# Kernel optimization log

Hardware: AMD Instinct MI355X
Metric: run time of the kernel (lower is better)

## Reference

```python
import jax, jax.numpy as jnp
import numpy as np

N = 2_097_152          # n_transitions = n_envs * buffer_size
GAMMA = 0.99
GAE_LAMBDA = 0.95
CLIP_EPS = 0.2
NORM_ADVANTAGES = True


def setup_inputs() -> dict:
    key = jax.random.key(0)
    ks = jax.random.split(key, 7)
    f = lambda k: jax.random.normal(k, (N, 1), dtype=jnp.float32)
    return {
        "rewards": f(ks[0]),
        "values": f(ks[1]),
        "next_values": f(ks[2]),
        "log_probs": -jnp.abs(f(ks[3])),       # log-probs are <= 0
        "old_log_probs": -jnp.abs(f(ks[4])),
        "terminated": jax.random.randint(ks[5], (N, 1), 0, 2).astype(bool),
        "truncated": jax.random.randint(ks[6], (N, 1), 0, 2).astype(bool),
    }


def reference(rewards, values, next_values, log_probs, old_log_probs,
              terminated, truncated):
    dtype = rewards.dtype
    dones = jnp.logical_or(terminated, truncated)
    not_term = 1.0 - terminated.astype(dtype)          # [N,1]
    not_done = 1.0 - dones.astype(dtype)               # [N,1]

    # TD residuals: delta_n = r_n + gamma * (1 - terminated_n) * V(s'_n) - V(s_n)
    deltas = rewards + GAMMA * not_term * next_values - values   # [N,1]

    # Reverse GAE recurrence (the torch Python for-loop, fused into one scan):
    # adv_n = (1 - done_n) * gamma * lambda * adv_{n+1} + delta_n
    coef = not_done[:, 0] * (GAMMA * GAE_LAMBDA)       # [N]

    def step(adv, cd):
        c, d = cd
        adv = c * adv + d
        return adv, adv

    _, advantages = jax.lax.scan(step, jnp.zeros((), dtype),
                                 (coef, deltas[:, 0]), reverse=True)
    advantages = advantages[:, None]                   # [N,1]

    lambda_returns = advantages + values               # [N,1]

    if NORM_ADVANTAGES:
        # torch .std() is the unbiased (ddof=1) estimator
        adv_n = (advantages - advantages.mean()) / (
            jnp.std(advantages, ddof=1) + 1e-9)
    else:
        adv_n = advantages

    # PPO clipped surrogate, per-sample (the .mean() is a trivial reduction)
    ratio = jnp.exp(log_probs - old_log_probs)
    clamped = jnp.clip(ratio, 1.0 - CLIP_EPS, 1.0 + CLIP_EPS)
    per_sample_actor_loss = -jnp.minimum(ratio * adv_n, clamped * adv_n)

    # [N,3]: normalized advantages, lambda returns, per-sample clipped objective
    return jnp.concatenate([adv_n, lambda_returns, per_sample_actor_loss], axis=1)
```

## Files before the change

kernel.cpp:

```cpp
#include <hip/hip_runtime.h>
#include <stdint.h>

static constexpr int BLOCK = 256;
static constexpr int ITEMS = 8;
static constexpr int CHUNK = BLOCK * ITEMS;
static constexpr int MAXNB = 1024;

#define GAMMA_F 0.99f
static __device__ __forceinline__ float gl_const() { return (float)(0.99 * 0.95); }

__device__ __forceinline__ int detect_mode(const void* term, int n_elems, int* flg) {
    int t = threadIdx.x;
    if (t == 0) { flg[0] = 0; flg[1] = 0; }
    __syncthreads();
    if (t < 256) {
        const unsigned char* p = (const unsigned char*)term;
        int i0 = 4 * t;
        if (i0 + 3 < n_elems) {
            unsigned b1 = p[i0 + 1], b2 = p[i0 + 2], b3 = p[i0 + 3];
            if (b1) atomicOr(&flg[0], 1);
            if (b2 | b3) atomicOr(&flg[1], 1);
        }
    }
    __syncthreads();
    return flg[0] ? 1 : (flg[1] ? 2 : 0);
}

__device__ __forceinline__ int load_bool1(const void* p, long i, int mode) {
    if (mode == 1) return ((const unsigned char*)p)[i] != 0;
    if (mode == 0) return ((const int*)p)[i] != 0;
    return ((const float*)p)[i] != 0.0f;
}

__device__ __forceinline__ void load_bool8(const void* p, long base, int mode, int* f) {
    if (mode == 1) {
        uint2 q = *(const uint2*)((const unsigned char*)p + base);
        unsigned w[2] = {q.x, q.y};
#pragma unroll
        for (int j = 0; j < 8; ++j) f[j] = (int)((w[j >> 2] >> ((j & 3) * 8)) & 0xffu);
    } else if (mode == 0) {
        const int4* q = (const int4*)((const int*)p + base);
#pragma unroll
        for (int k = 0; k < 2; ++k) {
            int4 v = q[k];
            f[4*k] = v.x; f[4*k+1] = v.y; f[4*k+2] = v.z; f[4*k+3] = v.w;
        }
    } else {
        const float4* q = (const float4*)((const float*)p + base);
#pragma unroll
        for (int k = 0; k < 2; ++k) {
            float4 v = q[k];
            f[4*k] = v.x != 0.f; f[4*k+1] = v.y != 0.f; f[4*k+2] = v.z != 0.f; f[4*k+3] = v.w != 0.f;
        }
    }
}

__device__ __forceinline__ void compute_cd(
    const float* __restrict__ rewards, const float* __restrict__ values,
    const float* __restrict__ next_values, const void* __restrict__ term,
    const void* __restrict__ trunc, int mode, long base, int n,
    float* c, float* d, float* v)
{
    const float GL = gl_const();
    if (base + ITEMS <= n) {
        float r[ITEMS], nv[ITEMS];
        const float4* r4 = (const float4*)(rewards + base);
        const float4* v4 = (const float4*)(values + base);
        const float4* n4 = (const float4*)(next_values + base);
#pragma unroll
        for (int k = 0; k < 2; ++k) {
            float4 a = r4[k]; r[4*k]=a.x; r[4*k+1]=a.y; r[4*k+2]=a.z; r[4*k+3]=a.w;
            float4 b = v4[k]; v[4*k]=b.x; v[4*k+1]=b.y; v[4*k+2]=b.z; v[4*k+3]=b.w;
            float4 q = n4[k]; nv[4*k]=q.x; nv[4*k+1]=q.y; nv[4*k+2]=q.z; nv[4*k+3]=q.w;
        }
        int tm[ITEMS], tr[ITEMS];
        load_bool8(term,  base, mode, tm);
        load_bool8(trunc, base, mode, tr);
#pragma unroll
        for (int j = 0; j < ITEMS; ++j) {
            float nt = tm[j] ? 0.f : 1.f;
            float nd = (tm[j] | tr[j]) ? 0.f : 1.f;
            d[j] = r[j] + GAMMA_F * nt * nv[j] - v[j];
            c[j] = nd * GL;
        }
    } else {
#pragma unroll
        for (int j = 0; j < ITEMS; ++j) {
            long i = base + j;
            if (i < (long)n) {
                int tm = load_bool1(term, i, mode);
                int tr = load_bool1(trunc, i, mode);
                float nt = tm ? 0.f : 1.f;
                float nd = (tm | tr) ? 0.f : 1.f;
                v[j] = values[i];
                d[j] = rewards[i] + GAMMA_F * nt * next_values[i] - v[j];
                c[j] = nd * GL;
            } else { c[j] = 1.f; d[j] = 0.f; v[j] = 0.f; }
        }
    }
}

__global__ __launch_bounds__(BLOCK) void k1_agg(
    const float* __restrict__ rewards, const float* __restrict__ values,
    const float* __restrict__ next_values, const void* __restrict__ term,
    const void* __restrict__ trunc, float2* __restrict__ blockAgg, int n)
{
    __shared__ int flg[2];
    __shared__ float sA[BLOCK], sB[BLOCK];
    int mode = detect_mode(term, n, flg);
    int t = threadIdx.x;
    long base = (long)blockIdx.x * CHUNK + (long)t * ITEMS;
    float c[ITEMS], d[ITEMS], v[ITEMS];
    compute_cd(rewards, values, next_values, term, trunc, mode, base, n, c, d, v);
    float a = 1.f, b = 0.f;
#pragma unroll
    for (int j = ITEMS - 1; j >= 0; --j) { b = c[j]*b + d[j]; a = c[j]*a; }
    sA[t] = a; sB[t] = b;
    __syncthreads();
    for (int dd = 1; dd < BLOCK; dd <<= 1) {
        float ra = 1.f, rb = 0.f;
        if (t + dd < BLOCK) { ra = sA[t + dd]; rb = sB[t + dd]; }
        __syncthreads();
        b = a * rb + b;
        a = a * ra;
        sA[t] = a; sB[t] = b;
        __syncthreads();
    }
    if (t == 0) blockAgg[blockIdx.x] = make_float2(a, b);
}

__global__ __launch_bounds__(BLOCK) void k2_scan(
    const float2* __restrict__ blockAgg, float* __restrict__ S, int nb)
{
    __shared__ float sA[BLOCK], sB[BLOCK];
    const int t = threadIdx.x;
    float la[4], lb[4];
#pragma unroll
    for (int j = 0; j < 4; ++j) {
        int i = 4 * t + j;
        if (i < nb) { float2 f = blockAgg[i]; la[j] = f.x; lb[j] = f.y; }
        else        { la[j] = 1.f; lb[j] = 0.f; }
    }
    float a = 1.f, b = 0.f;
#pragma unroll
    for (int j = 3; j >= 0; --j) { b = la[j] * b + lb[j]; a = la[j] * a; }
    sA[t] = a; sB[t] = b;
    __syncthreads();
    for (int dd = 1; dd < BLOCK; dd <<= 1) {
        float ra = 1.f, rb = 0.f;
        if (t + dd < BLOCK) { ra = sA[t + dd]; rb = sB[t + dd]; }
        __syncthreads();
        b = a * rb + b;
        a = a * ra;
        sA[t] = a; sB[t] = b;
        __syncthreads();
    }
    float x = (t + 1 < BLOCK) ? sB[t + 1] : 0.f;
    if (4 * t + 3 < nb) S[4 * t + 3] = x;
    x = la[3] * x + lb[3];
    if (4 * t + 2 < nb) S[4 * t + 2] = x;
    x = la[2] * x + lb[2];
    if (4 * t + 1 < nb) S[4 * t + 1] = x;
    x = la[1] * x + lb[1];
    if (4 * t     < nb) S[4 * t    ] = x;
}

__global__ __launch_bounds__(BLOCK) void k3_adv(
    const float* __restrict__ rewards, const float* __restrict__ values,
    const float* __restrict__ next_values, const void* __restrict__ term,
    const void* __restrict__ trunc, const float* __restrict__ S,
    float* __restrict__ advs, float2* __restrict__ blockSums, int n)
{
    __shared__ int flg[2];
    __shared__ float sA[BLOCK], sB[BLOCK];
    int mode = detect_mode(term, n, flg);
    int t = threadIdx.x;
    long base = (long)blockIdx.x * CHUNK + (long)t * ITEMS;
    float c[ITEMS], d[ITEMS], v[ITEMS];
    compute_cd(rewards, values, next_values, term, trunc, mode, base, n, c, d, v);
    float a = 1.f, b = 0.f;
#pragma unroll
    for (int j = ITEMS - 1; j >= 0; --j) { b = c[j]*b + d[j]; a = c[j]*a; }
    sA[t] = a; sB[t] = b;
    __syncthreads();
    for (int dd = 1; dd < BLOCK; dd <<= 1) {
        float ra = 1.f, rb = 0.f;
        if (t + dd < BLOCK) { ra = sA[t + dd]; rb = sB[t + dd]; }
        __syncthreads();
        b = a * rb + b;
        a = a * ra;
        sA[t] = a; sB[t] = b;
        __syncthreads();
    }
    float ea = 1.f, eb = 0.f;
    if (t + 1 < BLOCK) { ea = sA[t + 1]; eb = sB[t + 1]; }
    float x = ea * S[blockIdx.x] + eb;
    float adv[ITEMS];
    float s = 0.f, s2 = 0.f;
#pragma unroll
    for (int j = ITEMS - 1; j >= 0; --j) {
        x = c[j] * x + d[j];
        adv[j] = x;
        if (base + j < (long)n) { s += x; s2 += x * x; }
    }
    if (base + ITEMS <= n) {
        float4* dst = (float4*)(advs + base);
        dst[0] = make_float4(adv[0], adv[1], adv[2], adv[3]);
        dst[1] = make_float4(adv[4], adv[5], adv[6], adv[7]);
    } else {
        for (int j = 0; j < ITEMS; ++j)
            if (base + j < (long)n) advs[base + j] = adv[j];
    }
    __syncthreads();
    sA[t] = s; sB[t] = s2;
    __syncthreads();
    for (int dd = BLOCK / 2; dd > 0; dd >>= 1) {
        if (t < dd) { sA[t] += sA[t + dd]; sB[t] += sB[t + dd]; }
        __syncthreads();
    }
    if (t == 0) blockSums[blockIdx.x] = make_float2(sA[0], sB[0]);
}

__global__ __launch_bounds__(BLOCK) void k3b_stats(
    const float2* __restrict__ blockSums, float* __restrict__ stats, int nb, int n)
{
    __shared__ double dS[BLOCK], dS2[BLOCK];
    const int t = threadIdx.x;
    double s = 0.0, s2 = 0.0;
    for (int i = t; i < nb; i += BLOCK) {
        float2 f = blockSums[i];
        s += (double)f.x; s2 += (double)f.y;
    }
    dS[t] = s; dS2[t] = s2;
    __syncthreads();
    for (int dd = BLOCK / 2; dd > 0; dd >>= 1) {
        if (t < dd) { dS[t] += dS[t + dd]; dS2[t] += dS2[t + dd]; }
        __syncthreads();
    }
    if (t == 0) {
        double sum = dS[0], sumsq = dS2[0];
        double mean = sum / (double)n;
        double var = (sumsq - sum * sum / (double)n) / (double)(n - 1);
        if (var < 0.0) var = 0.0;
        stats[0] = (float)mean;
        stats[1] = 1.0f / ((float)sqrt(var) + 1e-9f);
    }
}

__global__ __launch_bounds__(BLOCK) void k4_final(
    const float* __restrict__ advs, const float* __restrict__ values,
    const float* __restrict__ lp, const float* __restrict__ olp,
    const float* __restrict__ stats, float* __restrict__ out, int n)
{
    long e = ((long)blockIdx.x * blockDim.x + threadIdx.x) * 4;
    if (e >= n) return;
    const float mean = stats[0];
    const float inv  = stats[1];
    if (e + 4 <= n) {
        float4 a4 = *(const float4*)(advs + e);
        float4 v4 = *(const float4*)(values + e);
        float4 l4 = *(const float4*)(lp + e);
        float4 o4 = *(const float4*)(olp + e);
        float av[4] = {a4.x, a4.y, a4.z, a4.w};
        float vv[4] = {v4.x, v4.y, v4.z, v4.w};
        float lv[4] = {l4.x, l4.y, l4.z, l4.w};
        float ov[4] = {o4.x, o4.y, o4.z, o4.w};
        float buf[12];
#pragma unroll
        for (int j = 0; j < 4; ++j) {
            float an = (av[j] - mean) * inv;
            float ratio = expf(lv[j] - ov[j]);
            float cl = fminf(fmaxf(ratio, 0.8f), 1.2f);
            buf[3*j]     = an;
            buf[3*j + 1] = av[j] + vv[j];
            buf[3*j + 2] = -fminf(ratio * an, cl * an);
        }
        float4* dst = (float4*)(out + 3 * e);
        dst[0] = make_float4(buf[0], buf[1], buf[2],  buf[3]);
        dst[1] = make_float4(buf[4], buf[5], buf[6],  buf[7]);
        dst[2] = make_float4(buf[8], buf[9], buf[10], buf[11]);
    } else {
        for (long i = e; i < (long)n; ++i) {
            float a = advs[i];
            float an = (a - mean) * inv;
            float ratio = expf(lp[i] - olp[i]);
            float cl = fminf(fmaxf(ratio, 0.8f), 1.2f);
            out[3*i]     = an;
            out[3*i + 1] = a + values[i];
            out[3*i + 2] = -fminf(ratio * an, cl * an);
        }
    }
}

extern "C" void kernel_launch(void* const* d_in, const int* in_sizes, int n_in,
                              void* d_out, int out_size, void* d_ws, size_t ws_size,
                              hipStream_t stream) {
    const float* rewards     = (const float*)d_in[0];
    const float* values      = (const float*)d_in[1];
    const float* next_values = (const float*)d_in[2];
    const float* lp          = (const float*)d_in[3];
    const float* olp         = (const float*)d_in[4];
    const void*  term        = d_in[5];
    const void*  trunc       = d_in[6];
    float* out = (float*)d_out;
    int n = in_sizes[0];
    int nb = (n + CHUNK - 1) / CHUNK;

    char* ws = (char*)d_ws;
    size_t advs_bytes = (((size_t)n * 4) + 255) & ~(size_t)255;
    float*  advs      = (float*)ws;
    float2* blockAgg  = (float2*)(ws + advs_bytes);
    float*  S         = (float*)(ws + advs_bytes + MAXNB * 8);
    float2* blockSums = (float2*)(ws + advs_bytes + MAXNB * 8 + MAXNB * 4);
    float*  stats     = (float*)(ws + advs_bytes + MAXNB * 8 + MAXNB * 4 + MAXNB * 8);

    k1_agg   <<<nb, BLOCK, 0, stream>>>(rewards, values, next_values, term, trunc, blockAgg, n);
    k2_scan  <<<1,  BLOCK, 0, stream>>>(blockAgg, S, nb);
    k3_adv   <<<nb, BLOCK, 0, stream>>>(rewards, values, next_values, term, trunc, S, advs, blockSums, n);
    k3b_stats<<<1,  BLOCK, 0, stream>>>(blockSums, stats, nb, n);
    int n4blocks = (int)(((long)n / 4 + BLOCK - 1) / BLOCK);
    k4_final <<<n4blocks, BLOCK, 0, stream>>>(advs, values, lp, olp, stats, out, n);
}
```

Baseline: 136.1 us.

## Compute advantage statistics algebraically in first pass and fuse finalize into scan

Each advantage is an affine function of its block's unknown carry-in (adv = p*x + q). The first pass therefore accumulates per-block sums of p, q, p², pq and q², and the single-block scan combines these with the resolved carries to get the global mean and variance in double precision. The separate advantage-write kernel, the stats kernel and the finalize kernel are merged into one pass that recomputes advantages in registers and writes the output directly. This removes the intermediate advantages buffer round-trip and two kernel launches. The cost is more per-thread arithmetic and shared-memory reductions, plus some risk of float precision loss in the expanded variance terms.

```diff
diff --git a/kernel.cpp b/kernel.cpp
--- a/kernel.cpp
+++ b/kernel.cpp
@@ -103,7 +103,123 @@
 __global__ __launch_bounds__(BLOCK) void k1_agg(
     const float* __restrict__ rewards, const float* __restrict__ values,
     const float* __restrict__ next_values, const void* __restrict__ term,
-    const void* __restrict__ trunc, float2* __restrict__ blockAgg, int n)
+    const void* __restrict__ trunc, float2* __restrict__ blockAgg,
+    float4* __restrict__ bs4, float* __restrict__ bs1, int n)
+{
+    __shared__ int flg[2];
+    __shared__ float sA[BLOCK], sB[BLOCK], sC[BLOCK], sD[BLOCK], sE[BLOCK];
+    int mode = detect_mode(term, n, flg);
+    int t = threadIdx.x;
+    long base = (long)blockIdx.x * CHUNK + (long)t * ITEMS;
+    float c[ITEMS], d[ITEMS], v[ITEMS];
+    compute_cd(rewards, values, next_values, term, trunc, mode, base, n, c, d, v);
+    float a = 1.f, b = 0.f;
+#pragma unroll
+    for (int j = ITEMS - 1; j >= 0; --j) { b = c[j]*b + d[j]; a = c[j]*a; }
+    sA[t] = a; sB[t] = b;
+    __syncthreads();
+    for (int dd = 1; dd < BLOCK; dd <<= 1) {
+        float ra = 1.f, rb = 0.f;
+        if (t + dd < BLOCK) { ra = sA[t + dd]; rb = sB[t + dd]; }
+        __syncthreads();
+        b = a * rb + b;
+        a = a * ra;
+        sA[t] = a; sB[t] = b;
+        __syncthreads();
+    }
+    float p = 1.f, q = 0.f;
+    if (t + 1 < BLOCK) { p = sA[t + 1]; q = sB[t + 1]; }
+    if (t == 0) blockAgg[blockIdx.x] = make_float2(a, b);
+    float sP = 0.f, sQ = 0.f, sP2 = 0.f, sPQ = 0.f, sQ2 = 0.f;
+#pragma unroll
+    for (int j = ITEMS - 1; j >= 0; --j) {
+        p = c[j] * p;
+        q = c[j] * q + d[j];
+        if (base + j < (long)n) {
+            sP += p; sQ += q; sP2 += p*p; sPQ += p*q; sQ2 += q*q;
+        }
+    }
+    __syncthreads();
+    sA[t] = sP; sB[t] = sQ; sC[t] = sP2; sD[t] = sPQ; sE[t] = sQ2;
+    __syncthreads();
+    for (int dd = BLOCK / 2; dd > 0; dd >>= 1) {
+        if (t < dd) {
+            sA[t] += sA[t + dd]; sB[t] += sB[t + dd]; sC[t] += sC[t + dd];
+            sD[t] += sD[t + dd]; sE[t] += sE[t + dd];
+        }
+        __syncthreads();
+    }
+    if (t == 0) {
+        bs4[blockIdx.x] = make_float4(sA[0], sB[0], sC[0], sD[0]);
+        bs1[blockIdx.x] = sE[0];
+    }
+}
+
+__global__ __launch_bounds__(BLOCK) void k2_scan(
+    const float2* __restrict__ blockAgg, const float4* __restrict__ bs4,
+    const float* __restrict__ bs1, float* __restrict__ S,
+    float* __restrict__ stats, int nb, int n)
+{
+    __shared__ float sA[BLOCK], sB[BLOCK];
+    __shared__ double dS[BLOCK], dS2[BLOCK];
+    const int t = threadIdx.x;
+    float la[4], lb[4];
+#pragma unroll
+    for (int j = 0; j < 4; ++j) {
+        int i = 4 * t + j;
+        if (i < nb) { float2 f = blockAgg[i]; la[j] = f.x; lb[j] = f.y; }
+        else        { la[j] = 1.f; lb[j] = 0.f; }
+    }
+    float a = 1.f, b = 0.f;
+#pragma unroll
+    for (int j = 3; j >= 0; --j) { b = la[j] * b + lb[j]; a = la[j] * a; }
+    sA[t] = a; sB[t] = b;
+    __syncthreads();
+    for (int dd = 1; dd < BLOCK; dd <<= 1) {
+        float ra = 1.f, rb = 0.f;
+        if (t + dd < BLOCK) { ra = sA[t + dd]; rb = sB[t + dd]; }
+        __syncthreads();
+        b = a * rb + b;
+        a = a * ra;
+        sA[t] = a; sB[t] = b;
+        __syncthreads();
+    }
+    float x = (t + 1 < BLOCK) ? sB[t + 1] : 0.f;
+    double ds = 0.0, ds2 = 0.0;
+#pragma unroll
+    for (int j = 3; j >= 0; --j) {
+        int i = 4 * t + j;
+        if (i < nb) {
+            S[i] = x;
+            float4 s4 = bs4[i];
+            double xd = (double)x;
+            ds  += (double)s4.x * xd + (double)s4.y;
+            ds2 += (double)s4.z * xd * xd + 2.0 * (double)s4.w * xd + (double)bs1[i];
+        }
+        x = la[j] * x + lb[j];
+    }
+    dS[t] = ds; dS2[t] = ds2;
+    __syncthreads();
+    for (int dd = BLOCK / 2; dd > 0; dd >>= 1) {
+        if (t < dd) { dS[t] += dS[t + dd]; dS2[t] += dS2[t + dd]; }
+        __syncthreads();
+    }
+    if (t == 0) {
+        double sum = dS[0], sumsq = dS2[0];
+        double mean = sum / (double)n;
+        double var = (sumsq - sum * sum / (double)n) / (double)(n - 1);
+        if (var < 0.0) var = 0.0;
+        stats[0] = (float)mean;
+        stats[1] = 1.0f / ((float)sqrt(var) + 1e-9f);
+    }
+}
+
+__global__ __launch_bounds__(BLOCK) void k3_final(
+    const float* __restrict__ rewards, const float* __restrict__ values,
+    const float* __restrict__ next_values, const void* __restrict__ term,
+    const void* __restrict__ trunc, const float* __restrict__ lp,
+    const float* __restrict__ olp, const float* __restrict__ S,
+    const float* __restrict__ stats, float* __restrict__ out, int n)
 {
     __shared__ int flg[2];
     __shared__ float sA[BLOCK], sB[BLOCK];
@@ -126,168 +242,51 @@
         sA[t] = a; sB[t] = b;
         __syncthreads();
     }
-    if (t == 0) blockAgg[blockIdx.x] = make_float2(a, b);
-}
-
-__global__ __launch_bounds__(BLOCK) void k2_scan(
-    const float2* __restrict__ blockAgg, float* __restrict__ S, int nb)
-{
-    __shared__ float sA[BLOCK], sB[BLOCK];
-    const int t = threadIdx.x;
-    float la[4], lb[4];
-#pragma unroll
-    for (int j = 0; j < 4; ++j) {
-        int i = 4 * t + j;
-        if (i < nb) { float2 f = blockAgg[i]; la[j] = f.x; lb[j] = f.y; }
-        else        { la[j] = 1.f; lb[j] = 0.f; }
-    }
-    float a = 1.f, b = 0.f;
-#pragma unroll
-    for (int j = 3; j >= 0; --j) { b = la[j] * b + lb[j]; a = la[j] * a; }
-    sA[t] = a; sB[t] = b;
-    __syncthreads();
-    for (int dd = 1; dd < BLOCK; dd <<= 1) {
-        float ra = 1.f, rb = 0.f;
-        if (t + dd < BLOCK) { ra = sA[t + dd]; rb = sB[t + dd]; }
-        __syncthreads();
-        b = a * rb + b;
-        a = a * ra;
-        sA[t] = a; sB[t] = b;
-        __syncthreads();
-    }
-    float x = (t + 1 < BLOCK) ? sB[t + 1] : 0.f;
-    if (4 * t + 3 < nb) S[4 * t + 3] = x;
-    x = la[3] * x + lb[3];
-    if (4 * t + 2 < nb) S[4 * t + 2] = x;
-    x = la[2] * x + lb[2];
-    if (4 * t + 1 < nb) S[4 * t + 1] = x;
-    x = la[1] * x + lb[1];
-    if (4 * t     < nb) S[4 * t    ] = x;
-}
-
-__global__ __launch_bounds__(BLOCK) void k3_adv(
-    const float* __restrict__ rewards, const float* __restrict__ values,
-    const float* __restrict__ next_values, const void* __restrict__ term,
-    const void* __restrict__ trunc, const float* __restrict__ S,
-    float* __restrict__ advs, float2* __restrict__ blockSums, int n)
-{
-    __shared__ int flg[2];
-    __shared__ float sA[BLOCK], sB[BLOCK];
-    int mode = detect_mode(term, n, flg);
-    int t = threadIdx.x;
-    long base = (long)blockIdx.x * CHUNK + (long)t * ITEMS;
-    float c[ITEMS], d[ITEMS], v[ITEMS];
-    compute_cd(rewards, values, next_values, term, trunc, mode, base, n, c, d, v);
-    float a = 1.f, b = 0.f;
-#pragma unroll
-    for (int j = ITEMS - 1; j >= 0; --j) { b = c[j]*b + d[j]; a = c[j]*a; }
-    sA[t] = a; sB[t] = b;
-    __syncthreads();
-    for (int dd = 1; dd < BLOCK; dd <<= 1) {
-        float ra = 1.f, rb = 0.f;
-        if (t + dd < BLOCK) { ra = sA[t + dd]; rb = sB[t + dd]; }
-        __syncthreads();
-        b = a * rb + b;
-        a = a * ra;
-        sA[t] = a; sB[t] = b;
-        __syncthreads();
-    }
     float ea = 1.f, eb = 0.f;
     if (t + 1 < BLOCK) { ea = sA[t + 1]; eb = sB[t + 1]; }
     float x = ea * S[blockIdx.x] + eb;
     float adv[ITEMS];
-    float s = 0.f, s2 = 0.f;
 #pragma unroll
     for (int j = ITEMS - 1; j >= 0; --j) {
         x = c[j] * x + d[j];
         adv[j] = x;
-        if (base + j < (long)n) { s += x; s2 += x * x; }
-    }
-    if (base + ITEMS <= n) {
-        float4* dst = (float4*)(advs + base);
-        dst[0] = make_float4(adv[0], adv[1], adv[2], adv[3]);
-        dst[1] = make_float4(adv[4], adv[5], adv[6], adv[7]);
-    } else {
-        for (int j = 0; j < ITEMS; ++j)
-            if (base + j < (long)n) advs[base + j] = adv[j];
-    }
-    __syncthreads();
-    sA[t] = s; sB[t] = s2;
-    __syncthreads();
-    for (int dd = BLOCK / 2; dd > 0; dd >>= 1) {
-        if (t < dd) { sA[t] += sA[t + dd]; sB[t] += sB[t + dd]; }
-        __syncthreads();
-    }
-    if (t == 0) blockSums[blockIdx.x] = make_float2(sA[0], sB[0]);
-}
-
-__global__ __launch_bounds__(BLOCK) void k3b_stats(
-    const float2* __restrict__ blockSums, float* __restrict__ stats, int nb, int n)
-{
-    __shared__ double dS[BLOCK], dS2[BLOCK];
-    const int t = threadIdx.x;
-    double s = 0.0, s2 = 0.0;
-    for (int i = t; i < nb; i += BLOCK) {
-        float2 f = blockSums[i];
-        s += (double)f.x; s2 += (double)f.y;
-    }
-    dS[t] = s; dS2[t] = s2;
-    __syncthreads();
-    for (int dd = BLOCK / 2; dd > 0; dd >>= 1) {
-        if (t < dd) { dS[t] += dS[t + dd]; dS2[t] += dS2[t + dd]; }
-        __syncthreads();
-    }
-    if (t == 0) {
-        double sum = dS[0], sumsq = dS2[0];
-        double mean = sum / (double)n;
-        double var = (sumsq - sum * sum / (double)n) / (double)(n - 1);
-        if (var < 0.0) var = 0.0;
-        stats[0] = (float)mean;
-        stats[1] = 1.0f / ((float)sqrt(var) + 1e-9f);
-    }
-}
-
-__global__ __launch_bounds__(BLOCK) void k4_final(
-    const float* __restrict__ advs, const float* __restrict__ values,
-    const float* __restrict__ lp, const float* __restrict__ olp,
-    const float* __restrict__ stats, float* __restrict__ out, int n)
-{
-    long e = ((long)blockIdx.x * blockDim.x + threadIdx.x) * 4;
-    if (e >= n) return;
+    }
     const float mean = stats[0];
     const float inv  = stats[1];
-    if (e + 4 <= n) {
-        float4 a4 = *(const float4*)(advs + e);
-        float4 v4 = *(const float4*)(values + e);
-        float4 l4 = *(const float4*)(lp + e);
-        float4 o4 = *(const float4*)(olp + e);
-        float av[4] = {a4.x, a4.y, a4.z, a4.w};
-        float vv[4] = {v4.x, v4.y, v4.z, v4.w};
-        float lv[4] = {l4.x, l4.y, l4.z, l4.w};
-        float ov[4] = {o4.x, o4.y, o4.z, o4.w};
-        float buf[12];
-#pragma unroll
-        for (int j = 0; j < 4; ++j) {
-            float an = (av[j] - mean) * inv;
-            float ratio = expf(lv[j] - ov[j]);
+    if (base + ITEMS <= n) {
+        float l[ITEMS], o[ITEMS];
+        const float4* l4 = (const float4*)(lp + base);
+        const float4* o4 = (const float4*)(olp + base);
+#pragma unroll
+        for (int k = 0; k < 2; ++k) {
+            float4 q = l4[k]; l[4*k]=q.x; l[4*k+1]=q.y; l[4*k+2]=q.z; l[4*k+3]=q.w;
+            float4 w = o4[k]; o[4*k]=w.x; o[4*k+1]=w.y; o[4*k+2]=w.z; o[4*k+3]=w.w;
+        }
+        float buf[3 * ITEMS];
+#pragma unroll
+        for (int j = 0; j < ITEMS; ++j) {
+            float an = (adv[j] - mean) * inv;
+            float ratio = expf(l[j] - o[j]);
             float cl = fminf(fmaxf(ratio, 0.8f), 1.2f);
             buf[3*j]     = an;
-            buf[3*j + 1] = av[j] + vv[j];
+            buf[3*j + 1] = adv[j] + v[j];
             buf[3*j + 2] = -fminf(ratio * an, cl * an);
         }
-        float4* dst = (float4*)(out + 3 * e);
-        dst[0] = make_float4(buf[0], buf[1], buf[2],  buf[3]);
-        dst[1] = make_float4(buf[4], buf[5], buf[6],  buf[7]);
-        dst[2] = make_float4(buf[8], buf[9], buf[10], buf[11]);
+        float4* dst = (float4*)(out + 3 * base);
+#pragma unroll
+        for (int k = 0; k < 6; ++k)
+            dst[k] = make_float4(buf[4*k], buf[4*k+1], buf[4*k+2], buf[4*k+3]);
     } else {
-        for (long i = e; i < (long)n; ++i) {
-            float a = advs[i];
-            float an = (a - mean) * inv;
-            float ratio = expf(lp[i] - olp[i]);
-            float cl = fminf(fmaxf(ratio, 0.8f), 1.2f);
-            out[3*i]     = an;
-            out[3*i + 1] = a + values[i];
-            out[3*i + 2] = -fminf(ratio * an, cl * an);
+        for (int j = 0; j < ITEMS; ++j) {
+            long i = base + j;
+            if (i < (long)n) {
+                float an = (adv[j] - mean) * inv;
+                float ratio = expf(lp[i] - olp[i]);
+                float cl = fminf(fmaxf(ratio, 0.8f), 1.2f);
+                out[3*i]     = an;
+                out[3*i + 1] = adv[j] + v[j];
+                out[3*i + 2] = -fminf(ratio * an, cl * an);
+            }
         }
     }
 }
@@ -307,17 +306,15 @@
     int nb = (n + CHUNK - 1) / CHUNK;
 
     char* ws = (char*)d_ws;
-    size_t advs_bytes = (((size_t)n * 4) + 255) & ~(size_t)255;
-    float*  advs      = (float*)ws;
-    float2* blockAgg  = (float2*)(ws + advs_bytes);
-    float*  S         = (float*)(ws + advs_bytes + MAXNB * 8);
-    float2* blockSums = (float2*)(ws + advs_bytes + MAXNB * 8 + MAXNB * 4);
-    float*  stats     = (float*)(ws + advs_bytes + MAXNB * 8 + MAXNB * 4 + MAXNB * 8);
-
-    k1_agg   <<<nb, BLOCK, 0, stream>>>(rewards, values, next_values, term, trunc, blockAgg, n);
-    k2_scan  <<<1,  BLOCK, 0, stream>>>(blockAgg, S, nb);
-    k3_adv   <<<nb, BLOCK, 0, stream>>>(rewards, values, next_values, term, trunc, S, advs, blockSums, n);
-    k3b_stats<<<1,  BLOCK, 0, stream>>>(blockSums, stats, nb, n);
-    int n4blocks = (int)(((long)n / 4 + BLOCK - 1) / BLOCK);
-    k4_final <<<n4blocks, BLOCK, 0, stream>>>(advs, values, lp, olp, stats, out, n);
-}
+    float2* blockAgg = (float2*)ws;
+    float4* bs4      = (float4*)(ws + MAXNB * 8);
+    float*  bs1      = (float*) (ws + MAXNB * 8 + MAXNB * 16);
+    float*  S        = (float*) (ws + MAXNB * 8 + MAXNB * 16 + MAXNB * 4);
+    float*  stats    = (float*) (ws + MAXNB * 8 + MAXNB * 16 + MAXNB * 4 + MAXNB * 4);
+
+    k1_agg <<<nb, BLOCK, 0, stream>>>(rewards, values, next_values, term, trunc,
+                                      blockAgg, bs4, bs1, n);
+    k2_scan<<<1,  BLOCK, 0, stream>>>(blockAgg, bs4, bs1, S, stats, nb, n);
+    k3_final<<<nb, BLOCK, 0, stream>>>(rewards, values, next_values, term, trunc,
+                                       lp, olp, S, stats, out, n);
+}
```

Result: faster. 130.9 us (-3.8%).
